# Optimization experiments

Measured on AMD Instinct MI355X. Metric: run time of the kernel, lower is better.

## Reference

```python
import jax, jax.numpy as jnp
import numpy as np
from jax import lax

# ---- constants mirroring Prediction.__init__ kwargs ----
INP = 608
NUM_CLASSES = 20
ALPHA, BETA = 1.0, 0.5
OBJ_T, CONF_T, LOC_T = 0.6, 0.05, 0.5
NMS_T, SIZE_T, SIGMA = 0.1, 0.0, 0.5
TOP_K = 8
M_CAND = 256          # fixed-size candidate cap for jit-compatible NMS
NEG = -1e9            # sentinel for masked scores
ANCHORS = [[(116, 90), (156, 198), (373, 326)],
           [(30, 61), (62, 45), (59, 119)],
           [(10, 13), (16, 30), (33, 23)]]


def _decode(pred, anchors):
    """pred: (B, A, G, G, 6+C) raw level output -> decoded flat tensors."""
    B, A, G, _, C = pred.shape
    stride = INP // G
    xy = jax.nn.sigmoid(pred[..., 0:2])
    g = jnp.arange(G, dtype=pred.dtype)
    gx, gy = jnp.meshgrid(g, g)                      # gx[i,j]=j, gy[i,j]=i (np.meshgrid 'xy')
    off = jnp.stack([gx, gy], axis=-1)[None, None]   # (1,1,G,G,2)
    xy = ALPHA * xy - 0.5 * (ALPHA - 1.0) + off
    anc = jnp.asarray(anchors, dtype=pred.dtype) / stride  # (A,2) scaled to grid units
    wh = jnp.exp(pred[..., 2:4]) * anc[None, :, None, None, :]
    box = jnp.concatenate([xy, wh], axis=-1) * stride       # back to pixel units
    obj = jax.nn.sigmoid(pred[..., 4])
    loc = jax.nn.sigmoid(pred[..., 5])
    clsp = jax.nn.softmax(pred[..., 6:], axis=-1)
    N = A * G * G
    return (box.reshape(B, N, 4), obj.reshape(B, N),
            loc.reshape(B, N), clsp.reshape(B, N, NUM_CLASSES))


def _soft_nms(boxes, s0, cls):
    """Per-image Gaussian soft-NMS (class-aware), +1 pixel IoU convention as in bbox_iou.
    boxes: (M,4) xyxy, s0: (M,) scores (NEG for invalid), cls: (M,) int. Returns kept mask."""
    M = s0.shape[0]

    def step(carry, _):
        s, kept = carry
        j = jnp.argmax(s)
        do = s[j] >= NMS_T
        kept = kept | ((jnp.arange(M) == j) & do)
        bj = boxes[j]
        ix1 = jnp.maximum(bj[0], boxes[:, 0]); iy1 = jnp.maximum(bj[1], boxes[:, 1])
        ix2 = jnp.minimum(bj[2], boxes[:, 2]); iy2 = jnp.minimum(bj[3], boxes[:, 3])
        inter = jnp.maximum(ix2 - ix1 + 1.0, 0.0) * jnp.maximum(iy2 - iy1 + 1.0, 0.0)
        a1 = (bj[2] - bj[0] + 1.0) * (bj[3] - bj[1] + 1.0)
        a2 = (boxes[:, 2] - boxes[:, 0] + 1.0) * (boxes[:, 3] - boxes[:, 1] + 1.0)
        iou = inter / (a1 + a2 - inter + 1e-16)
        decay = jnp.exp(-(iou * iou) / SIGMA)
        s_new = jnp.where(cls == cls[j], s * decay, s).at[j].set(NEG)
        s = jnp.where(do, s_new, s)
        return (s, kept), None

    (_, kept), _ = lax.scan(step, (s0, jnp.zeros(M, dtype=bool)), None, length=M)
    return kept


def _forward(pred_l0, pred_l1, pred_l2):
    parts = [_decode(p, a) for p, a in zip([pred_l0, pred_l1, pred_l2], ANCHORS)]
    box = jnp.concatenate([p[0] for p in parts], axis=1)   # (B,N,4) xywh
    obj = jnp.concatenate([p[1] for p in parts], axis=1)
    loc = jnp.concatenate([p[2] for p in parts], axis=1)
    clsp = jnp.concatenate([p[3] for p in parts], axis=1)

    cx, cy, w, h = box[..., 0], box[..., 1], box[..., 2], box[..., 3]
    x1 = jnp.clip(cx - w / 2, 0.0, INP); y1 = jnp.clip(cy - h / 2, 0.0, INP)
    x2 = jnp.clip(cx + w / 2, 0.0, INP); y2 = jnp.clip(cy + h / 2, 0.0, INP)
    boxes = jnp.stack([x1, y1, x2, y2], axis=-1)            # (B,N,4) xyxy, clamped

    cls_conf = jnp.max(clsp, axis=-1)
    cls_id = jnp.argmax(clsp, axis=-1)
    area = (x2 - x1) * (y2 - y1)
    valid = ((obj >= OBJ_T) & (area >= INP * INP * SIZE_T)
             & (obj * cls_conf >= CONF_T) & (loc >= LOC_T))
    score = (obj * cls_conf) ** BETA * loc ** (1.0 - BETA)
    masked = jnp.where(valid, score, NEG)

    # fixed-size candidate set per image (descending-score sort + cap)
    vals, idx = lax.top_k(masked, M_CAND)                   # (B,M)
    cboxes = jnp.take_along_axis(boxes, idx[..., None], axis=1)
    ccls = jnp.take_along_axis(cls_id, idx, axis=1)
    s0 = jnp.where(vals > NEG / 2, vals, NEG)

    kept = jax.vmap(_soft_nms)(cboxes, s0, ccls)            # (B,M) bool

    # keep_top_k: top_k among kept, ranked by ORIGINAL (pre-decay) score
    fscore = jnp.where(kept, vals, NEG)
    fvals, fidx = lax.top_k(fscore, TOP_K)                  # (B,TOP_K)
    fboxes = jnp.take_along_axis(cboxes, fidx[..., None], axis=1)
    fcls = jnp.take_along_axis(ccls, fidx, axis=1)
    row = jnp.concatenate([fboxes, fvals[..., None],
                           fcls[..., None].astype(fboxes.dtype)], axis=-1)  # (B,K,6)
    ok = fvals > NEG / 2
    return jnp.where(ok[..., None], row, 0.0)


def setup_inputs() -> dict:
    key = jax.random.key(0)
    k0, k1, k2 = jax.random.split(key, 3)
    return {
        "pred_l0": jax.random.normal(k0, (64, 3, 19, 19, 26), dtype=jnp.float32),
        "pred_l1": jax.random.normal(k1, (64, 3, 38, 38, 26), dtype=jnp.float32),
        "pred_l2": jax.random.normal(k2, (64, 3, 76, 76, 26), dtype=jnp.float32),
    }


def reference(pred_l0, pred_l1, pred_l2):
    return _forward(pred_l0, pred_l1, pred_l2)
```

## Files before the change

### kernel.cpp

```cpp
#include <hip/hip_runtime.h>
#include <climits>

constexpr int kB  = 64;
constexpr int kG0 = 19, kG1 = 38, kG2 = 76;
constexpr int kN0 = 3 * kG0 * kG0;
constexpr int kN1 = 3 * kG1 * kG1;
constexpr int kN2 = 3 * kG2 * kG2;
constexpr int kN  = kN0 + kN1 + kN2;
constexpr int kM  = 256;
constexpr int kTopK = 8;
constexpr float kNEG = -1e9f;

constexpr int kT0 = 5, kT1 = 17, kT2 = 68;
constexpr int kTilesPerImg = kT0 + kT1 + kT2;

__constant__ float c_anchors[3][3][2] = {
    {{116.f, 90.f}, {156.f, 198.f}, {373.f, 326.f}},
    {{30.f, 61.f},  {62.f, 45.f},   {59.f, 119.f}},
    {{10.f, 13.f},  {16.f, 30.f},   {33.f, 23.f}},
};

__device__ __forceinline__ float sigm(float x) { return 1.0f / (1.0f + expf(-x)); }

__device__ __forceinline__ unsigned score_to_key(float s) {
  unsigned fb = __float_as_uint(s);
  unsigned m = (fb & 0x80000000u) ? 0xFFFFFFFFu : 0x80000000u;
  return fb ^ m;
}
__device__ __forceinline__ float key_to_score(unsigned k) {
  unsigned fb = (k & 0x80000000u) ? (k ^ 0x80000000u) : ~k;
  return __uint_as_float(fb);
}

__device__ __forceinline__ const float* cell_ptr(
    const float* p0, const float* p1, const float* p2, int b, int n,
    int& lvl, int& a, int& gi, int& gj, float& stride) {
  const float* src; int G, m;
  if (n < kN0)            { src = p0; G = kG0; lvl = 0; m = n;             stride = 32.f; }
  else if (n < kN0 + kN1) { src = p1; G = kG1; lvl = 1; m = n - kN0;       stride = 16.f; }
  else                    { src = p2; G = kG2; lvl = 2; m = n - kN0 - kN1; stride = 8.f; }
  int gg = G * G;
  a = m / gg;
  int r = m - a * gg;
  gi = r / G;
  gj = r - gi * G;
  return src + (size_t)((((b * 3 + a) * G + gi) * G + gj)) * 26;
}

__device__ __forceinline__ void waveArgmax(float& v, int& i) {
  #pragma unroll
  for (int off = 1; off < 64; off <<= 1) {
    float ov = __shfl_xor(v, off);
    int oi = __shfl_xor(i, off);
    if (ov > v || (ov == v && oi < i)) { v = ov; i = oi; }
  }
}
__device__ __forceinline__ float waveMax(float v) {
  #pragma unroll
  for (int off = 1; off < 64; off <<= 1) v = fmaxf(v, __shfl_xor(v, off));
  return v;
}
__device__ __forceinline__ float sel4f(const float a[4], int q) {
  float r = a[0];
  r = (q == 1) ? a[1] : r;
  r = (q == 2) ? a[2] : r;
  r = (q == 3) ? a[3] : r;
  return r;
}
__device__ __forceinline__ int sel4i(const int a[4], int q) {
  int r = a[0];
  r = (q == 1) ? a[1] : r;
  r = (q == 2) ? a[2] : r;
  r = (q == 3) ? a[3] : r;
  return r;
}

__global__ __launch_bounds__(256) void score_kernel(
    const float* __restrict__ p0, const float* __restrict__ p1, const float* __restrict__ p2,
    unsigned* __restrict__ keys)
{
  __shared__ float2 lds2[256 * 13];

  int t = threadIdx.x;
  int blk = blockIdx.x;
  int b = blk / kTilesPerImg;
  int r = blk - b * kTilesPerImg;
  const float* slab; int NL, lvlOff, tile;
  if (r < kT0)             { slab = p0; NL = kN0; lvlOff = 0;          tile = r; }
  else if (r < kT0 + kT1)  { slab = p1; NL = kN1; lvlOff = kN0;        tile = r - kT0; }
  else                     { slab = p2; NL = kN2; lvlOff = kN0 + kN1;  tile = r - kT0 - kT1; }
  int cellBase = tile * 256;
  int nc = min(256, NL - cellBase);

  const float2* g2 = (const float2*)(slab + ((size_t)b * NL + cellBase) * 26);
  int totF2 = nc * 13;
  for (int i = t; i < totF2; i += 256) lds2[i] = g2[i];
  __syncthreads();

  if (t < nc) {
    const float2* c2 = &lds2[t * 13];
    float2 ol = c2[2];
    float obj = sigm(ol.x);
    float loc = sigm(ol.y);
    float tch[20];
    #pragma unroll
    for (int j = 0; j < 10; ++j) { float2 v = c2[3 + j]; tch[2*j] = v.x; tch[2*j+1] = v.y; }
    float lm = tch[0];
    #pragma unroll
    for (int c = 1; c < 20; ++c) lm = fmaxf(lm, tch[c]);
    float se = 0.f;
    #pragma unroll
    for (int c = 0; c < 20; ++c) se += expf(tch[c] - lm);
    float cls_conf = 1.0f / se;
    float conf = obj * cls_conf;
    float masked = (obj >= 0.6f && loc >= 0.5f && conf >= 0.05f)
                   ? sqrtf(conf) * sqrtf(loc) : kNEG;
    keys[(size_t)b * kN + lvlOff + cellBase + t] = score_to_key(masked);
  }
}

__device__ __forceinline__ void findThresholdBin(
    const int* hist, int NB, int needed,
    int& outB, int& outCumAbove, int& outTotal,
    int* shWave, int* shOut)
{
  int tid = threadIdx.x, lane = tid & 63, w = tid >> 6;
  if (tid == 0) { shOut[0] = -1; shOut[1] = 0; }
  int ipt = (NB + 511) / 512;
  int base = tid * ipt;
  int csum = 0;
  for (int i = 0; i < ipt; ++i) { int bn = base + i; if (bn < NB) csum += hist[bn]; }
  int v = csum;
  #pragma unroll
  for (int off = 1; off < 64; off <<= 1) {
    int tv = __shfl_down(v, off);
    if (lane + off < 64) v += tv;
  }
  if (lane == 0) shWave[w] = v;
  __syncthreads();
  int above = 0, total = 0;
  #pragma unroll
  for (int q = 0; q < 8; ++q) {
    int wt = shWave[q];
    total += wt;
    if (q > w) above += wt;
  }
  int S = v + above;
  if (S >= needed && S - csum < needed) {
    int running = S - csum;
    for (int i = ipt - 1; i >= 0; --i) {
      int bn = base + i; if (bn >= NB) continue;
      int c = hist[bn];
      if (running + c >= needed) { shOut[0] = bn; shOut[1] = running; break; }
      running += c;
    }
  }
  __syncthreads();
  outB = shOut[0]; outCumAbove = shOut[1]; outTotal = total;
  __syncthreads();
}

__global__ __launch_bounds__(512) void select_kernel(
    const unsigned* __restrict__ keys, int* __restrict__ candIdx)
{
  int b = blockIdx.x, tid = threadIdx.x;
  const unsigned* kk = keys + (size_t)b * kN;
  const unsigned keyNEG = score_to_key(kNEG);

  __shared__ int hist[4096];
  __shared__ int eqBuf[1024];
  __shared__ int shWave[8], shOut[2];
  __shared__ unsigned sT;
  __shared__ int sCgt;

  for (int i = tid; i < 4096; i += 512) hist[i] = 0;
  __syncthreads();
  for (int x = tid; x < kN; x += 512) {
    unsigned k = kk[x];
    if (k >= 0x80000000u) atomicAdd(&hist[k >> 20], 1);
  }
  __syncthreads();
  int B, cumAbove1, total1;
  findThresholdBin(hist, 4096, kM, B, cumAbove1, total1, shWave, shOut);

  if (total1 < kM) {
    if (tid == 0) { sT = keyNEG; sCgt = total1; }
    __syncthreads();
  } else {
    int needed2 = kM - cumAbove1;
    for (int i = tid; i < 4096; i += 512) hist[i] = 0;
    __syncthreads();
    for (int x = tid; x < kN; x += 512) {
      unsigned k = kk[x];
      if ((int)(k >> 20) == B) atomicAdd(&hist[(k >> 8) & 0xFFF], 1);
    }
    __syncthreads();
    int B2, cumAbove2, total2;
    findThresholdBin(hist, 4096, needed2, B2, cumAbove2, total2, shWave, shOut);
    int prefix24 = (B << 12) | B2;
    int needed3 = needed2 - cumAbove2;

    for (int i = tid; i < 256; i += 512) hist[i] = 0;
    __syncthreads();
    for (int x = tid; x < kN; x += 512) {
      unsigned k = kk[x];
      if ((int)(k >> 8) == prefix24) atomicAdd(&hist[k & 0xFF], 1);
    }
    __syncthreads();
    int B3, cumAbove3, total3;
    findThresholdBin(hist, 256, needed3, B3, cumAbove3, total3, shWave, shOut);
    if (tid == 0) {
      sT = ((unsigned)prefix24 << 8) | (unsigned)B3;
      sCgt = cumAbove1 + cumAbove2 + cumAbove3;
    }
    __syncthreads();
  }

  unsigned T = sT;
  int cgt = sCgt;

  __shared__ int sCnt, eqCnt;
  if (tid == 0) { sCnt = 0; eqCnt = 0; }
  __syncthreads();
  int* ci = candIdx + (size_t)b * kM;
  for (int x = tid; x < kN; x += 512) {
    unsigned k = kk[x];
    if (k > T) { int p = atomicAdd(&sCnt, 1); ci[p] = x; }
    else if (k == T && T != keyNEG) { int p = atomicAdd(&eqCnt, 1); if (p < 1024) eqBuf[p] = x; }
  }
  __syncthreads();

  int needed = kM - cgt;
  if (T == keyNEG) {
    if (tid >= cgt && tid < kM) ci[tid] = -1;
  } else {
    int ce = min(eqCnt, 1024);
    if (ce == needed) {
      if (tid < needed) ci[cgt + tid] = eqBuf[tid];
    } else if (tid == 0) {
      for (int q = 0; q < needed; ++q) {
        int mv = INT_MAX, mp = 0;
        for (int x = 0; x < ce; ++x) if (eqBuf[x] < mv) { mv = eqBuf[x]; mp = x; }
        ci[cgt + q] = mv; eqBuf[mp] = INT_MAX;
      }
    }
  }
}

__global__ __launch_bounds__(64) void nms_kernel(
    const float* __restrict__ p0, const float* __restrict__ p1, const float* __restrict__ p2,
    const unsigned* __restrict__ keys, const int* __restrict__ candIdx,
    float* __restrict__ out)
{
  int b = blockIdx.x, lane = threadIdx.x;

  float x1[4], y1[4], x2[4], y2[4], val[4], s[4];
  int cls[4];
  bool kept[4];

  #pragma unroll
  for (int q = 0; q < 4; ++q) {
    int n = candIdx[(size_t)b * kM + q * 64 + lane];
    kept[q] = false;
    x1[q] = y1[q] = x2[q] = y2[q] = 0.f;
    cls[q] = 0; val[q] = kNEG; s[q] = kNEG;
    if (n >= 0) {
      float sc = key_to_score(keys[(size_t)b * kN + n]);
      val[q] = sc; s[q] = sc;
      int lvl, a, gi, gj; float stride;
      const float* p = cell_ptr(p0, p1, p2, b, n, lvl, a, gi, gj, stride);
      const float2* r2 = (const float2*)p;
      float2 c01 = r2[0], c23 = r2[1];
      float cx = (sigm(c01.x) + (float)gj) * stride;
      float cy = (sigm(c01.y) + (float)gi) * stride;
      float w = expf(c23.x) * c_anchors[lvl][a][0];
      float h = expf(c23.y) * c_anchors[lvl][a][1];
      x1[q] = fminf(fmaxf(cx - 0.5f * w, 0.f), 608.f);
      y1[q] = fminf(fmaxf(cy - 0.5f * h, 0.f), 608.f);
      x2[q] = fminf(fmaxf(cx + 0.5f * w, 0.f), 608.f);
      y2[q] = fminf(fmaxf(cy + 0.5f * h, 0.f), 608.f);
      float lm = -3.4e38f; int mc = 0;
      #pragma unroll
      for (int j = 3; j < 13; ++j) {
        float2 v = r2[j];
        int c0 = 2 * (j - 3);
        if (v.x > lm) { lm = v.x; mc = c0; }
        if (v.y > lm) { lm = v.y; mc = c0 + 1; }
      }
      cls[q] = mc;
    }
  }

  float top8[8];
  #pragma unroll
  for (int i = 0; i < 8; ++i) top8[i] = kNEG;
  int keptCount = 0;

  for (int it = 0; it < kM; ++it) {
    float bv = s[0]; int bq = 0;
    #pragma unroll
    for (int q = 1; q < 4; ++q) if (s[q] > bv) { bv = s[q]; bq = q; }
    int bi = bq * 64 + lane;
    waveArgmax(bv, bi);
    if (bv < 0.1f) break;

    int wlane = bi & 63, wq = bi >> 6;
    float jx1 = __shfl(sel4f(x1, wq), wlane);
    float jy1 = __shfl(sel4f(y1, wq), wlane);
    float jx2 = __shfl(sel4f(x2, wq), wlane);
    float jy2 = __shfl(sel4f(y2, wq), wlane);
    float jval = __shfl(sel4f(val, wq), wlane);
    int   cj  = __shfl(sel4i(cls, wq), wlane);

    float a1 = (jx2 - jx1 + 1.0f) * (jy2 - jy1 + 1.0f);
    #pragma unroll
    for (int q = 0; q < 4; ++q) {
      if (cls[q] == cj) {
        float ix1 = fmaxf(jx1, x1[q]), iy1 = fmaxf(jy1, y1[q]);
        float ix2 = fminf(jx2, x2[q]), iy2 = fminf(jy2, y2[q]);
        float inter = fmaxf(ix2 - ix1 + 1.0f, 0.0f) * fmaxf(iy2 - iy1 + 1.0f, 0.0f);
        float a2 = (x2[q] - x1[q] + 1.0f) * (y2[q] - y1[q] + 1.0f);
        float iou = inter / (a1 + a2 - inter + 1e-16f);
        s[q] *= expf(-(iou * iou) / 0.5f);
      }
      if (bi == q * 64 + lane) { kept[q] = true; s[q] = kNEG; }
    }

    float v = jval;
    #pragma unroll
    for (int i = 0; i < 8; ++i) { float m = fmaxf(top8[i], v); v = fminf(top8[i], v); top8[i] = m; }
    ++keptCount;
    if (keptCount >= kTopK) {
      float am = kNEG;
      #pragma unroll
      for (int q = 0; q < 4; ++q) if (s[q] >= 0.1f) am = fmaxf(am, val[q]);
      am = waveMax(am);
      if (am < top8[7]) break;
    }
  }

  float f[4];
  #pragma unroll
  for (int q = 0; q < 4; ++q) f[q] = kept[q] ? val[q] : kNEG;
  for (int k = 0; k < kTopK; ++k) {
    float bv = f[0]; int bq = 0;
    #pragma unroll
    for (int q = 1; q < 4; ++q) if (f[q] > bv) { bv = f[q]; bq = q; }
    int bi = bq * 64 + lane;
    waveArgmax(bv, bi);
    int wlane = bi & 63, wq = bi >> 6;
    if (lane == wlane) {
      float* o = out + (size_t)(b * kTopK + k) * 6;
      if (bv > kNEG * 0.5f) {
        o[0] = sel4f(x1, wq); o[1] = sel4f(y1, wq);
        o[2] = sel4f(x2, wq); o[3] = sel4f(y2, wq);
        o[4] = sel4f(val, wq); o[5] = (float)sel4i(cls, wq);
      } else {
        o[0] = 0.f; o[1] = 0.f; o[2] = 0.f; o[3] = 0.f; o[4] = 0.f; o[5] = 0.f;
      }
    }
    #pragma unroll
    for (int q = 0; q < 4; ++q) if (bi == q * 64 + lane) f[q] = kNEG;
  }
}

extern "C" void kernel_launch(void* const* d_in, const int* in_sizes, int n_in,
                              void* d_out, int out_size, void* d_ws, size_t ws_size,
                              hipStream_t stream) {
  const float* p0 = (const float*)d_in[0];
  const float* p1 = (const float*)d_in[1];
  const float* p2 = (const float*)d_in[2];
  float* out = (float*)d_out;

  unsigned* keys = (unsigned*)d_ws;
  int* candIdx = (int*)(keys + (size_t)kB * kN);

  score_kernel<<<kB * kTilesPerImg, 256, 0, stream>>>(p0, p1, p2, keys);
  select_kernel<<<kB, 512, 0, stream>>>(keys, candIdx);
  nms_kernel<<<kB, 64, 0, stream>>>(p0, p1, p2, keys, candIdx, out);
}
```

Measured before the change: 271.3 us.

## Compact passing candidates into key/index pairs and async-load tiles to LDS

The score kernel now appends only cells that pass the objectness/loc/conf thresholds as packed (key,index) 64-bit pairs through a per-image atomic counter. The select kernel then scans only those compacted entries instead of every cell four times, and passes candidate keys on directly so NMS no longer reads the full key array. Tile loads for the two larger levels use global_load_lds async copies. Fast __expf and rcp intrinsics replace the precise exp and division. This adds a zero kernel launch and global atomics, and the order of equal-key entries now depends on atomic ordering, although ties are still broken by smallest index.

Result: slower. 395.4 us (+45.7%).

```diff
diff --git a/kernel.cpp b/kernel.cpp
--- a/kernel.cpp
+++ b/kernel.cpp
@@ -20,7 +20,9 @@
     {{10.f, 13.f},  {16.f, 30.f},   {33.f, 23.f}},
 };
 
-__device__ __forceinline__ float sigm(float x) { return 1.0f / (1.0f + expf(-x)); }
+__device__ __forceinline__ float fexpf(float x) { return __expf(x); }
+__device__ __forceinline__ float frcpf(float x) { return __builtin_amdgcn_rcpf(x); }
+__device__ __forceinline__ float fsigm(float x) { return frcpf(1.0f + __expf(-x)); }
 
 __device__ __forceinline__ unsigned score_to_key(float s) {
   unsigned fb = __float_as_uint(s);
@@ -75,9 +77,19 @@
   return r;
 }
 
+__device__ __forceinline__ void async_copy16(const void* g, void* s) {
+  __builtin_amdgcn_global_load_lds(
+      (__attribute__((address_space(1))) unsigned int*)g,
+      (__attribute__((address_space(3))) unsigned int*)s, 16, 0, 0);
+}
+
+__global__ void zero_kernel(int* __restrict__ cnt) {
+  if ((int)threadIdx.x < kB) cnt[threadIdx.x] = 0;
+}
+
 __global__ __launch_bounds__(256) void score_kernel(
     const float* __restrict__ p0, const float* __restrict__ p1, const float* __restrict__ p2,
-    unsigned* __restrict__ keys)
+    unsigned long long* __restrict__ pairs, int* __restrict__ cnt)
 {
   __shared__ float2 lds2[256 * 13];
 
@@ -85,23 +97,39 @@
   int blk = blockIdx.x;
   int b = blk / kTilesPerImg;
   int r = blk - b * kTilesPerImg;
-  const float* slab; int NL, lvlOff, tile;
-  if (r < kT0)             { slab = p0; NL = kN0; lvlOff = 0;          tile = r; }
+  const float* slab; int NL, lvlOff, tile; bool lvl0 = false;
+  if (r < kT0)             { slab = p0; NL = kN0; lvlOff = 0;          tile = r;             lvl0 = true; }
   else if (r < kT0 + kT1)  { slab = p1; NL = kN1; lvlOff = kN0;        tile = r - kT0; }
   else                     { slab = p2; NL = kN2; lvlOff = kN0 + kN1;  tile = r - kT0 - kT1; }
   int cellBase = tile * 256;
   int nc = min(256, NL - cellBase);
-
-  const float2* g2 = (const float2*)(slab + ((size_t)b * NL + cellBase) * 26);
-  int totF2 = nc * 13;
-  for (int i = t; i < totF2; i += 256) lds2[i] = g2[i];
+  const float* gbase = slab + ((size_t)b * NL + cellBase) * 26;
+
+  if (!lvl0 && nc == 256) {
+    int wave = t >> 6, lane = t & 63;
+    const char* gc = (const char*)gbase;
+    char* sc = (char*)lds2;
+    #pragma unroll
+    for (int c = 0; c < 6; ++c) {
+      int off = c * 4096 + wave * 1024;
+      async_copy16(gc + off + lane * 16, sc + off);
+    }
+    if (wave < 2) {
+      int off = 24576 + wave * 1024;
+      async_copy16(gc + off + lane * 16, sc + off);
+    }
+  } else {
+    const float2* g2 = (const float2*)gbase;
+    int tot = nc * 13;
+    for (int i = t; i < tot; i += 256) lds2[i] = g2[i];
+  }
   __syncthreads();
 
   if (t < nc) {
     const float2* c2 = &lds2[t * 13];
     float2 ol = c2[2];
-    float obj = sigm(ol.x);
-    float loc = sigm(ol.y);
+    float obj = fsigm(ol.x);
+    float loc = fsigm(ol.y);
     float tch[20];
     #pragma unroll
     for (int j = 0; j < 10; ++j) { float2 v = c2[3 + j]; tch[2*j] = v.x; tch[2*j+1] = v.y; }
@@ -110,12 +138,16 @@
     for (int c = 1; c < 20; ++c) lm = fmaxf(lm, tch[c]);
     float se = 0.f;
     #pragma unroll
-    for (int c = 0; c < 20; ++c) se += expf(tch[c] - lm);
-    float cls_conf = 1.0f / se;
+    for (int c = 0; c < 20; ++c) se += fexpf(tch[c] - lm);
+    float cls_conf = frcpf(se);
     float conf = obj * cls_conf;
-    float masked = (obj >= 0.6f && loc >= 0.5f && conf >= 0.05f)
-                   ? sqrtf(conf) * sqrtf(loc) : kNEG;
-    keys[(size_t)b * kN + lvlOff + cellBase + t] = score_to_key(masked);
+    if (obj >= 0.6f && loc >= 0.5f && conf >= 0.05f) {
+      float score = sqrtf(conf) * sqrtf(loc);
+      int n = lvlOff + cellBase + t;
+      int pos = atomicAdd(&cnt[b], 1);
+      pairs[(size_t)b * kN + pos] =
+          ((unsigned long long)score_to_key(score) << 32) | (unsigned)n;
+    }
   }
 }
 
@@ -161,10 +193,12 @@
 }
 
 __global__ __launch_bounds__(512) void select_kernel(
-    const unsigned* __restrict__ keys, int* __restrict__ candIdx)
+    const unsigned long long* __restrict__ pairs, const int* __restrict__ cnt,
+    int* __restrict__ candIdx, unsigned* __restrict__ candKey)
 {
   int b = blockIdx.x, tid = threadIdx.x;
-  const unsigned* kk = keys + (size_t)b * kN;
+  const unsigned long long* kk = pairs + (size_t)b * kN;
+  int NC = cnt[b];
   const unsigned keyNEG = score_to_key(kNEG);
 
   __shared__ int hist[4096];
@@ -175,10 +209,8 @@
 
   for (int i = tid; i < 4096; i += 512) hist[i] = 0;
   __syncthreads();
-  for (int x = tid; x < kN; x += 512) {
-    unsigned k = kk[x];
-    if (k >= 0x80000000u) atomicAdd(&hist[k >> 20], 1);
-  }
+  for (int x = tid; x < NC; x += 512)
+    atomicAdd(&hist[(unsigned)(kk[x] >> 52)], 1);
   __syncthreads();
   int B, cumAbove1, total1;
   findThresholdBin(hist, 4096, kM, B, cumAbove1, total1, shWave, shOut);
@@ -190,8 +222,8 @@
     int needed2 = kM - cumAbove1;
     for (int i = tid; i < 4096; i += 512) hist[i] = 0;
     __syncthreads();
-    for (int x = tid; x < kN; x += 512) {
-      unsigned k = kk[x];
+    for (int x = tid; x < NC; x += 512) {
+      unsigned k = (unsigned)(kk[x] >> 32);
       if ((int)(k >> 20) == B) atomicAdd(&hist[(k >> 8) & 0xFFF], 1);
     }
     __syncthreads();
@@ -202,8 +234,8 @@
 
     for (int i = tid; i < 256; i += 512) hist[i] = 0;
     __syncthreads();
-    for (int x = tid; x < kN; x += 512) {
-      unsigned k = kk[x];
+    for (int x = tid; x < NC; x += 512) {
+      unsigned k = (unsigned)(kk[x] >> 32);
       if ((int)(k >> 8) == prefix24) atomicAdd(&hist[k & 0xFF], 1);
     }
     __syncthreads();
@@ -223,25 +255,31 @@
   if (tid == 0) { sCnt = 0; eqCnt = 0; }
   __syncthreads();
   int* ci = candIdx + (size_t)b * kM;
-  for (int x = tid; x < kN; x += 512) {
-    unsigned k = kk[x];
-    if (k > T) { int p = atomicAdd(&sCnt, 1); ci[p] = x; }
-    else if (k == T && T != keyNEG) { int p = atomicAdd(&eqCnt, 1); if (p < 1024) eqBuf[p] = x; }
+  unsigned* ck = candKey + (size_t)b * kM;
+  for (int x = tid; x < NC; x += 512) {
+    unsigned long long v = kk[x];
+    unsigned k = (unsigned)(v >> 32);
+    if (k > T) {
+      int p = atomicAdd(&sCnt, 1);
+      ci[p] = (int)(unsigned)v; ck[p] = k;
+    } else if (k == T && T != keyNEG) {
+      int p = atomicAdd(&eqCnt, 1); if (p < 1024) eqBuf[p] = (int)(unsigned)v;
+    }
   }
   __syncthreads();
 
   int needed = kM - cgt;
   if (T == keyNEG) {
-    if (tid >= cgt && tid < kM) ci[tid] = -1;
+    if (tid >= cgt && tid < kM) { ci[tid] = -1; ck[tid] = keyNEG; }
   } else {
     int ce = min(eqCnt, 1024);
     if (ce == needed) {
-      if (tid < needed) ci[cgt + tid] = eqBuf[tid];
+      if (tid < needed) { ci[cgt + tid] = eqBuf[tid]; ck[cgt + tid] = T; }
     } else if (tid == 0) {
       for (int q = 0; q < needed; ++q) {
         int mv = INT_MAX, mp = 0;
         for (int x = 0; x < ce; ++x) if (eqBuf[x] < mv) { mv = eqBuf[x]; mp = x; }
-        ci[cgt + q] = mv; eqBuf[mp] = INT_MAX;
+        ci[cgt + q] = mv; ck[cgt + q] = T; eqBuf[mp] = INT_MAX;
       }
     }
   }
@@ -249,7 +287,7 @@
 
 __global__ __launch_bounds__(64) void nms_kernel(
     const float* __restrict__ p0, const float* __restrict__ p1, const float* __restrict__ p2,
-    const unsigned* __restrict__ keys, const int* __restrict__ candIdx,
+    const int* __restrict__ candIdx, const unsigned* __restrict__ candKey,
     float* __restrict__ out)
 {
   int b = blockIdx.x, lane = threadIdx.x;
@@ -260,21 +298,21 @@
 
   #pragma unroll
   for (int q = 0; q < 4; ++q) {
-    int n = candIdx[(size_t)b * kM + q * 64 + lane];
+    int slot = b * kM + q * 64 + lane;
+    int n = candIdx[slot];
+    float sc = key_to_score(candKey[slot]);
     kept[q] = false;
     x1[q] = y1[q] = x2[q] = y2[q] = 0.f;
-    cls[q] = 0; val[q] = kNEG; s[q] = kNEG;
+    cls[q] = 0; val[q] = sc; s[q] = sc;
     if (n >= 0) {
-      float sc = key_to_score(keys[(size_t)b * kN + n]);
-      val[q] = sc; s[q] = sc;
       int lvl, a, gi, gj; float stride;
       const float* p = cell_ptr(p0, p1, p2, b, n, lvl, a, gi, gj, stride);
       const float2* r2 = (const float2*)p;
       float2 c01 = r2[0], c23 = r2[1];
-      float cx = (sigm(c01.x) + (float)gj) * stride;
-      float cy = (sigm(c01.y) + (float)gi) * stride;
-      float w = expf(c23.x) * c_anchors[lvl][a][0];
-      float h = expf(c23.y) * c_anchors[lvl][a][1];
+      float cx = (fsigm(c01.x) + (float)gj) * stride;
+      float cy = (fsigm(c01.y) + (float)gi) * stride;
+      float w = fexpf(c23.x) * c_anchors[lvl][a][0];
+      float h = fexpf(c23.y) * c_anchors[lvl][a][1];
       x1[q] = fminf(fmaxf(cx - 0.5f * w, 0.f), 608.f);
       y1[q] = fminf(fmaxf(cy - 0.5f * h, 0.f), 608.f);
       x2[q] = fminf(fmaxf(cx + 0.5f * w, 0.f), 608.f);
@@ -321,7 +359,7 @@
         float inter = fmaxf(ix2 - ix1 + 1.0f, 0.0f) * fmaxf(iy2 - iy1 + 1.0f, 0.0f);
         float a2 = (x2[q] - x1[q] + 1.0f) * (y2[q] - y1[q] + 1.0f);
         float iou = inter / (a1 + a2 - inter + 1e-16f);
-        s[q] *= expf(-(iou * iou) / 0.5f);
+        s[q] *= fexpf(-(iou * iou) * 2.0f);
       }
       if (bi == q * 64 + lane) { kept[q] = true; s[q] = kNEG; }
     }
@@ -372,10 +410,13 @@
   const float* p2 = (const float*)d_in[2];
   float* out = (float*)d_out;
 
-  unsigned* keys = (unsigned*)d_ws;
-  int* candIdx = (int*)(keys + (size_t)kB * kN);
-
-  score_kernel<<<kB * kTilesPerImg, 256, 0, stream>>>(p0, p1, p2, keys);
-  select_kernel<<<kB, 512, 0, stream>>>(keys, candIdx);
-  nms_kernel<<<kB, 64, 0, stream>>>(p0, p1, p2, keys, candIdx, out);
-}
+  unsigned long long* pairs = (unsigned long long*)d_ws;
+  int* candIdx = (int*)(pairs + (size_t)kB * kN);
+  unsigned* candKey = (unsigned*)(candIdx + kB * kM);
+  int* cnt = (int*)(candKey + kB * kM);
+
+  zero_kernel<<<1, 64, 0, stream>>>(cnt);
+  score_kernel<<<kB * kTilesPerImg, 256, 0, stream>>>(p0, p1, p2, pairs, cnt);
+  select_kernel<<<kB, 512, 0, stream>>>(pairs, cnt, candIdx, candKey);
+  nms_kernel<<<kB, 64, 0, stream>>>(p0, p1, p2, candIdx, candKey, out);
+}
```
